# Performance work log

Measured on AMD Instinct MI355X. Metric: run time of the kernel, lower is better.

The kernel has to match this reference:

```python
import jax, jax.numpy as jnp
import numpy as np

B, S, E, H = 8, 1024, 1024, 16
D = E // H


def setup_inputs() -> dict:
    key = jax.random.key(0)
    ks = jax.random.split(key, 5)
    s = 1.0 / np.sqrt(E)
    return {
        "hidden_states": jax.random.normal(ks[0], (B, S, E), dtype=jnp.float32),
        "w_q": jax.random.normal(ks[1], (E, E), dtype=jnp.float32) * s,
        "w_k": jax.random.normal(ks[2], (E, E), dtype=jnp.float32) * s,
        "w_v": jax.random.normal(ks[3], (E, E), dtype=jnp.float32) * s,
        "w_out": jax.random.normal(ks[4], (E, E), dtype=jnp.float32) * s,
        "b_out": jnp.zeros((E,), dtype=jnp.float32),
    }


def reference(hidden_states, w_q, w_k, w_v, w_out, b_out):
    b, s = hidden_states.shape[0], hidden_states.shape[1]
    # Linear projections (weights stored as [in, out] = torch W^T)
    q = hidden_states @ w_q
    k = hidden_states @ w_k
    v = hidden_states @ w_v
    # Faithful to the original: raw reshape (B,S,E)->(B,H,S,D), NOT a head-split transpose
    q = q.reshape(b, H, s, D)
    k = k.reshape(b, H, s, D)
    v = v.reshape(b, H, s, D)
    # Scores scaled by embedding_size**-0.5 (original quirk, not head_dim**-0.5)
    scores = jnp.einsum("bhsd,bhtd->bhst", q, k) * (E ** -0.5)
    attn = jax.nn.softmax(scores, axis=-1)
    out = jnp.einsum("bhst,bhtd->bhsd", attn, v)  # [B,H,S,D]
    out = out.transpose(0, 2, 1, 3).reshape(b, s, E)  # [B,S,E]
    return out @ w_out + b_out
```

## Files before the change

### kernel.cpp

```cpp
#include <hip/hip_runtime.h>
#include <hip/hip_bf16.h>
#include <stdint.h>
#include <stddef.h>

static constexpr int Bb = 8, Ss = 1024, Ee = 1024, Hh = 16, Dd = 64;
static constexpr int Mm = Bb * Ss;

typedef __attribute__((ext_vector_type(8))) short frag8;
typedef __attribute__((ext_vector_type(4))) float fx4;
typedef __attribute__((ext_vector_type(4))) short s4v;

#define GP(p) ((const __attribute__((address_space(1))) void*)(p))
#define LP(p) ((__attribute__((address_space(3))) void*)(p))

static constexpr float QSC = 0.045084220027780106f;

__device__ inline short f2bf(float x) {
  union { float f; unsigned u; } c; c.f = x;
  unsigned u = c.u;
  unsigned r = (u + 0x7FFFu + ((u >> 16) & 1u)) >> 16;
  return (short)r;
}

__global__ __launch_bounds__(256) void cvt_kernel(const float* __restrict__ in,
                                                  short* __restrict__ out, int n4) {
  int i = blockIdx.x * 256 + threadIdx.x;
  if (i >= n4) return;
  float4 v = *((const float4*)in + i);
  union { short s[4]; uint2 u; } o;
  o.s[0] = f2bf(v.x); o.s[1] = f2bf(v.y); o.s[2] = f2bf(v.z); o.s[3] = f2bf(v.w);
  *(uint2*)(out + (size_t)i * 4) = o.u;
}

__global__ __launch_bounds__(256) void transpose_cvt4(const float* __restrict__ w0,
                                                      const float* __restrict__ w1,
                                                      const float* __restrict__ w2,
                                                      const float* __restrict__ w3,
                                                      short* __restrict__ WtBase) {
  __shared__ short tile[32][33];
  const int z = blockIdx.z;
  const float* W = z == 0 ? w0 : (z == 1 ? w1 : (z == 2 ? w2 : w3));
  short* Wt = WtBase + (size_t)z * 1024 * 1024;
  const int bx = blockIdx.x * 32;
  const int by = blockIdx.y * 32;
  const int tx = threadIdx.x & 31, ty = threadIdx.x >> 5;
  #pragma unroll
  for (int j = 0; j < 32; j += 8)
    tile[ty + j][tx] = f2bf(W[(size_t)(by + ty + j) * 1024 + bx + tx]);
  __syncthreads();
  #pragma unroll
  for (int j = 0; j < 32; j += 8)
    Wt[(size_t)(bx + ty + j) * 1024 + by + tx] = tile[tx][ty + j];
}

__global__ __launch_bounds__(256) void transpose_v(const short* __restrict__ V,
                                                   short* __restrict__ Vt) {
  __shared__ short tile[64][65];
  const int bh = blockIdx.y;
  const int s0 = blockIdx.x * 64;
  const short* Vb = V + (size_t)bh * 65536;
  short* Vtb = Vt + (size_t)bh * 65536;
  const int tx = threadIdx.x & 63, ty = threadIdx.x >> 6;
  #pragma unroll
  for (int j = 0; j < 64; j += 4)
    tile[ty + j][tx] = Vb[(size_t)(s0 + ty + j) * 64 + tx];
  __syncthreads();
  #pragma unroll
  for (int j = 0; j < 64; j += 4)
    Vtb[(size_t)(ty + j) * 1024 + s0 + tx] = tile[tx][ty + j];
}

template <int MODE>
__global__ __launch_bounds__(256) void gemm_bt(const short* __restrict__ A,
                                               const short* __restrict__ Bt,
                                               void* __restrict__ C0,
                                               void* __restrict__ C1,
                                               void* __restrict__ C2,
                                               const float* __restrict__ bias,
                                               int M, int N, int K) {
  __shared__ short As[128 * 32];
  __shared__ short Bs[128 * 32];
  const int t = threadIdx.x;
  const int w = t >> 6, lane = t & 63;
  const int fm = lane & 15, quad = lane >> 4;
  const int m0 = blockIdx.y * 128, n0 = blockIdx.x * 128;
  const int wm = (w >> 1) * 64, wn = (w & 1) * 64;
  fx4 acc[4][4];
  #pragma unroll
  for (int i = 0; i < 4; ++i)
    #pragma unroll
    for (int j = 0; j < 4; ++j) acc[i][j] = (fx4){0.f, 0.f, 0.f, 0.f};

  for (int k0 = 0; k0 < K; k0 += 32) {
    #pragma unroll
    for (int i = 0; i < 2; ++i) {
      int chunk = i * 256 + t;
      int row = chunk >> 2, cc = chunk & 3;
      __builtin_amdgcn_global_load_lds(GP(A + (size_t)(m0 + row) * K + k0 + cc * 8),
                                       LP(As + chunk * 8), 16, 0, 0);
      __builtin_amdgcn_global_load_lds(GP(Bt + (size_t)(n0 + row) * K + k0 + cc * 8),
                                       LP(Bs + chunk * 8), 16, 0, 0);
    }
    __syncthreads();
    frag8 af[4], bf[4];
    #pragma unroll
    for (int mt = 0; mt < 4; ++mt)
      af[mt] = *(const frag8*)(As + (wm + mt * 16 + fm) * 32 + quad * 8);
    #pragma unroll
    for (int nt = 0; nt < 4; ++nt)
      bf[nt] = *(const frag8*)(Bs + (wn + nt * 16 + fm) * 32 + quad * 8);
    #pragma unroll
    for (int mt = 0; mt < 4; ++mt)
      #pragma unroll
      for (int nt = 0; nt < 4; ++nt)
        acc[mt][nt] = __builtin_amdgcn_mfma_f32_16x16x32_bf16(af[mt], bf[nt], acc[mt][nt], 0, 0, 0);
    __syncthreads();
  }
  if (MODE == 0) {
    const int nb = n0 >> 10;
    short* dst = nb == 0 ? (short*)C0 : (nb == 1 ? (short*)C1 : (short*)C2);
    const float scl = (nb == 0) ? QSC : 1.0f;
    const int nl0 = n0 & 1023;
    #pragma unroll
    for (int mt = 0; mt < 4; ++mt)
      #pragma unroll
      for (int nt = 0; nt < 4; ++nt)
        #pragma unroll
        for (int r = 0; r < 4; ++r) {
          int row = m0 + wm + mt * 16 + quad * 4 + r;
          int col = nl0 + wn + nt * 16 + fm;
          dst[(size_t)row * 1024 + col] = f2bf(acc[mt][nt][r] * scl);
        }
  } else {
    #pragma unroll
    for (int mt = 0; mt < 4; ++mt)
      #pragma unroll
      for (int nt = 0; nt < 4; ++nt)
        #pragma unroll
        for (int r = 0; r < 4; ++r) {
          int row = m0 + wm + mt * 16 + quad * 4 + r;
          int col = n0 + wn + nt * 16 + fm;
          ((float*)C0)[(size_t)row * N + col] = acc[mt][nt][r] + bias[col];
        }
  }
}

__global__ __launch_bounds__(256, 2) void attn_kernel(const short* __restrict__ Q,
                                                      const short* __restrict__ K,
                                                      const short* __restrict__ Vt,
                                                      short* __restrict__ Ctx) {
  __shared__ short Ks[4096];
  __shared__ short Vs[4096];
  __shared__ short Plds[4 * 64 * 72];
  const int bh = blockIdx.x, qt = blockIdx.y;
  const int t = threadIdx.x;
  const int w = t >> 6, lane = t & 63;
  const int fm = lane & 15, quad = lane >> 4;
  const short* Qb = Q + (size_t)bh * 65536;
  const short* Kb = K + (size_t)bh * 65536;
  const short* Vb = Vt + (size_t)bh * 65536;
  const int q0 = qt * 256 + w * 64;
  short* myP = Plds + w * 4608;

  frag8 qb[4][2];
  #pragma unroll
  for (int g = 0; g < 4; ++g)
    #pragma unroll
    for (int h = 0; h < 2; ++h)
      qb[g][h] = *(const frag8*)(Qb + (size_t)(q0 + g * 16 + fm) * 64 + h * 32 + quad * 8);

  fx4 O[4][4];
  #pragma unroll
  for (int g = 0; g < 4; ++g)
    #pragma unroll
    for (int nt = 0; nt < 4; ++nt) O[g][nt] = (fx4){0.f, 0.f, 0.f, 0.f};
  float lp[4] = {0.f, 0.f, 0.f, 0.f};

  int koff[2], voff[2], loff[2];
  #pragma unroll
  for (int i = 0; i < 2; ++i) {
    int c = i * 256 + t;
    int cf = c & 15, cq = (c >> 4) & 3, ch = (c >> 6) & 1, cg = c >> 7;
    koff[i] = (cg * 16 + cf) * 64 + ch * 32 + cq * 8;
    voff[i] = (cg * 16 + cf) * 1024 + ch * 32 + cq * 8;
    loff[i] = c * 8;
  }

  for (int c = 0; c < 16; ++c) {
    const int key0 = c * 64;
    #pragma unroll
    for (int i = 0; i < 2; ++i) {
      __builtin_amdgcn_global_load_lds(GP(Kb + (size_t)key0 * 64 + koff[i]),
                                       LP(Ks + loff[i]), 16, 0, 0);
      __builtin_amdgcn_global_load_lds(GP(Vb + (size_t)key0 + voff[i]),
                                       LP(Vs + loff[i]), 16, 0, 0);
    }
    __syncthreads();

    #pragma unroll
    for (int s = 0; s < 4; ++s) {
      frag8 k0 = *(const frag8*)(Ks + (s * 2 + 0) * 512 + lane * 8);
      frag8 k1 = *(const frag8*)(Ks + (s * 2 + 1) * 512 + lane * 8);
      #pragma unroll
      for (int g = 0; g < 4; ++g) {
        fx4 z = (fx4){0.f, 0.f, 0.f, 0.f};
        z = __builtin_amdgcn_mfma_f32_16x16x32_bf16(k0, qb[g][0], z, 0, 0, 0);
        z = __builtin_amdgcn_mfma_f32_16x16x32_bf16(k1, qb[g][1], z, 0, 0, 0);
        s4v pv;
        #pragma unroll
        for (int r = 0; r < 4; ++r) {
          float p = __builtin_amdgcn_exp2f(z[r]);
          lp[g] += p;
          union { float f; unsigned u; } cv; cv.f = p;
          pv[r] = (short)(cv.u >> 16);
        }
        *(s4v*)(myP + (g * 16 + fm) * 72 + s * 16 + quad * 4) = pv;
      }
    }
    asm volatile("s_waitcnt lgkmcnt(0)" ::: "memory");
    #pragma unroll
    for (int h = 0; h < 2; ++h) {
      frag8 pf[4];
      #pragma unroll
      for (int g = 0; g < 4; ++g)
        pf[g] = *(const frag8*)(myP + (g * 16 + fm) * 72 + h * 32 + quad * 8);
      #pragma unroll
      for (int nt = 0; nt < 4; ++nt) {
        frag8 vf = *(const frag8*)(Vs + (nt * 2 + h) * 512 + lane * 8);
        #pragma unroll
        for (int g = 0; g < 4; ++g)
          O[g][nt] = __builtin_amdgcn_mfma_f32_16x16x32_bf16(pf[g], vf, O[g][nt], 0, 0, 0);
      }
    }
    __syncthreads();
  }

  float rl[4][4];
  #pragma unroll
  for (int g = 0; g < 4; ++g) {
    float v = lp[g];
    v += __shfl_xor(v, 16, 64);
    v += __shfl_xor(v, 32, 64);
    float inv = 1.f / v;
    #pragma unroll
    for (int r = 0; r < 4; ++r) rl[g][r] = __shfl(inv, quad * 4 + r, 16);
  }
  const int b = bh >> 4, h = bh & 15;
  #pragma unroll
  for (int g = 0; g < 4; ++g)
    #pragma unroll
    for (int nt = 0; nt < 4; ++nt)
      #pragma unroll
      for (int r = 0; r < 4; ++r) {
        int row = b * 1024 + q0 + g * 16 + quad * 4 + r;
        int col = h * 64 + nt * 16 + fm;
        Ctx[(size_t)row * 1024 + col] = f2bf(O[g][nt][r] * rl[g][r]);
      }
}

extern "C" void kernel_launch(void* const* d_in, const int* in_sizes, int n_in,
                              void* d_out, int out_size, void* d_ws, size_t ws_size,
                              hipStream_t stream) {
  const float* hs = (const float*)d_in[0];
  const float* wq = (const float*)d_in[1];
  const float* wk = (const float*)d_in[2];
  const float* wv = (const float*)d_in[3];
  const float* wo = (const float*)d_in[4];
  const float* bo = (const float*)d_in[5];
  float* out = (float*)d_out;

  char* wp = (char*)d_ws;
  const size_t MB16 = (size_t)Mm * Ee * 2;
  const size_t MB2  = (size_t)Ee * Ee * 2;
  short* Xb  = (short*)wp; wp += MB16;
  short* Wqt = (short*)wp; wp += MB2;
  short* Wkt = (short*)wp; wp += MB2;
  short* Wvt = (short*)wp; wp += MB2;
  short* Wot = (short*)wp; wp += MB2;
  short* Qb  = (short*)wp; wp += MB16;
  short* Kb  = (short*)wp; wp += MB16;
  short* Vb  = (short*)wp; wp += MB16;
  short* Vt  = (short*)wp; wp += MB16;
  short* Ctx = (short*)wp; wp += MB16;

  cvt_kernel<<<(Mm * Ee / 4 + 255) / 256, 256, 0, stream>>>(hs, Xb, Mm * Ee / 4);
  transpose_cvt4<<<dim3(32, 32, 4), 256, 0, stream>>>(wq, wk, wv, wo, Wqt);
  gemm_bt<0><<<dim3(24, 64), 256, 0, stream>>>(Xb, Wqt, Qb, Kb, Vb, nullptr, Mm, 3072, Ee);
  transpose_v<<<dim3(16, 128), 256, 0, stream>>>(Vb, Vt);
  attn_kernel<<<dim3(128, 4), 256, 0, stream>>>(Qb, Kb, Vt, Ctx);
  gemm_bt<1><<<dim3(8, 64), 256, 0, stream>>>(Ctx, Wot, out, nullptr, nullptr, bo, Mm, Ee, Ee);
}
```

Baseline: 249.4 us.

## Fuse prep kernels, write V transposed from GEMM epilogue, remap blocks per XCD

Merges the input conversion and weight transpose kernels into one launch, and removes the separate V transpose by having the QKV GEMM epilogue scatter V directly into the transposed layout used by attention. It also swizzles GEMM block indices so that each XCD handles a contiguous range of N tiles, which should improve L2 reuse of the weight tiles. The aim is to cut launch overhead and one full read/write pass over V. The trade-off is that the V stores in the epilogue are strided scatter writes, which coalesce less well.

After: 353.2 us. +41.6%, slower.

```diff
diff --git a/kernel.cpp b/kernel.cpp
--- a/kernel.cpp
+++ b/kernel.cpp
@@ -22,27 +22,29 @@
   return (short)r;
 }
 
-__global__ __launch_bounds__(256) void cvt_kernel(const float* __restrict__ in,
-                                                  short* __restrict__ out, int n4) {
-  int i = blockIdx.x * 256 + threadIdx.x;
-  if (i >= n4) return;
-  float4 v = *((const float4*)in + i);
-  union { short s[4]; uint2 u; } o;
-  o.s[0] = f2bf(v.x); o.s[1] = f2bf(v.y); o.s[2] = f2bf(v.z); o.s[3] = f2bf(v.w);
-  *(uint2*)(out + (size_t)i * 4) = o.u;
-}
-
-__global__ __launch_bounds__(256) void transpose_cvt4(const float* __restrict__ w0,
-                                                      const float* __restrict__ w1,
-                                                      const float* __restrict__ w2,
-                                                      const float* __restrict__ w3,
-                                                      short* __restrict__ WtBase) {
+__global__ __launch_bounds__(256) void prep_kernel(const float* __restrict__ hs,
+                                                   short* __restrict__ Xb,
+                                                   const float* __restrict__ w0,
+                                                   const float* __restrict__ w1,
+                                                   const float* __restrict__ w2,
+                                                   const float* __restrict__ w3,
+                                                   short* __restrict__ WtBase) {
   __shared__ short tile[32][33];
-  const int z = blockIdx.z;
+  const int id = blockIdx.x;
+  if (id < 8192) {
+    int i = id * 256 + threadIdx.x;
+    float4 v = *((const float4*)hs + i);
+    union { short s[4]; uint2 u; } o;
+    o.s[0] = f2bf(v.x); o.s[1] = f2bf(v.y); o.s[2] = f2bf(v.z); o.s[3] = f2bf(v.w);
+    *(uint2*)(Xb + (size_t)i * 4) = o.u;
+    return;
+  }
+  const int id2 = id - 8192;
+  const int z = id2 >> 10, t10 = id2 & 1023;
   const float* W = z == 0 ? w0 : (z == 1 ? w1 : (z == 2 ? w2 : w3));
   short* Wt = WtBase + (size_t)z * 1024 * 1024;
-  const int bx = blockIdx.x * 32;
-  const int by = blockIdx.y * 32;
+  const int bx = (t10 & 31) * 32;
+  const int by = (t10 >> 5) * 32;
   const int tx = threadIdx.x & 31, ty = threadIdx.x >> 5;
   #pragma unroll
   for (int j = 0; j < 32; j += 8)
@@ -51,23 +53,6 @@
   #pragma unroll
   for (int j = 0; j < 32; j += 8)
     Wt[(size_t)(bx + ty + j) * 1024 + by + tx] = tile[tx][ty + j];
-}
-
-__global__ __launch_bounds__(256) void transpose_v(const short* __restrict__ V,
-                                                   short* __restrict__ Vt) {
-  __shared__ short tile[64][65];
-  const int bh = blockIdx.y;
-  const int s0 = blockIdx.x * 64;
-  const short* Vb = V + (size_t)bh * 65536;
-  short* Vtb = Vt + (size_t)bh * 65536;
-  const int tx = threadIdx.x & 63, ty = threadIdx.x >> 6;
-  #pragma unroll
-  for (int j = 0; j < 64; j += 4)
-    tile[ty + j][tx] = Vb[(size_t)(s0 + ty + j) * 64 + tx];
-  __syncthreads();
-  #pragma unroll
-  for (int j = 0; j < 64; j += 4)
-    Vtb[(size_t)(ty + j) * 1024 + s0 + tx] = tile[tx][ty + j];
 }
 
 template <int MODE>
@@ -83,7 +68,10 @@
   const int t = threadIdx.x;
   const int w = t >> 6, lane = t & 63;
   const int fm = lane & 15, quad = lane >> 4;
-  const int m0 = blockIdx.y * 128, n0 = blockIdx.x * 128;
+  const int lin = blockIdx.x;
+  const int xcd = lin & 7, kk = lin >> 3;
+  const int m_t = kk & 63, nloc = kk >> 6;
+  const int m0 = m_t * 128, n0 = (xcd * (N >> 10) + nloc) * 128;
   const int wm = (w >> 1) * 64, wn = (w & 1) * 64;
   fx4 acc[4][4];
   #pragma unroll
@@ -118,19 +106,40 @@
   }
   if (MODE == 0) {
     const int nb = n0 >> 10;
-    short* dst = nb == 0 ? (short*)C0 : (nb == 1 ? (short*)C1 : (short*)C2);
-    const float scl = (nb == 0) ? QSC : 1.0f;
     const int nl0 = n0 & 1023;
-    #pragma unroll
-    for (int mt = 0; mt < 4; ++mt)
-      #pragma unroll
-      for (int nt = 0; nt < 4; ++nt)
-        #pragma unroll
-        for (int r = 0; r < 4; ++r) {
-          int row = m0 + wm + mt * 16 + quad * 4 + r;
-          int col = nl0 + wn + nt * 16 + fm;
-          dst[(size_t)row * 1024 + col] = f2bf(acc[mt][nt][r] * scl);
+    if (nb == 2) {
+      short* Vt = (short*)C2;
+      #pragma unroll
+      for (int mt = 0; mt < 4; ++mt) {
+        const int row = m0 + wm + mt * 16 + quad * 4;
+        const int b = row >> 10;
+        const int h = (row >> 6) & 15;
+        const int s_low = row & 63;
+        #pragma unroll
+        for (int nt = 0; nt < 4; ++nt) {
+          const int e = nl0 + wn + nt * 16 + fm;
+          const int d = e & 63;
+          const int sp_hi = e >> 6;
+          const size_t base = (size_t)(b * 16 + h) * 65536 + (size_t)d * 1024 + sp_hi;
+          #pragma unroll
+          for (int r = 0; r < 4; ++r)
+            Vt[base + (size_t)(s_low + r) * 16] = f2bf(acc[mt][nt][r]);
         }
+      }
+    } else {
+      short* dst = nb == 0 ? (short*)C0 : (short*)C1;
+      const float scl = (nb == 0) ? QSC : 1.0f;
+      #pragma unroll
+      for (int mt = 0; mt < 4; ++mt)
+        #pragma unroll
+        for (int nt = 0; nt < 4; ++nt)
+          #pragma unroll
+          for (int r = 0; r < 4; ++r) {
+            int row = m0 + wm + mt * 16 + quad * 4 + r;
+            int col = nl0 + wn + nt * 16 + fm;
+            dst[(size_t)row * 1024 + col] = f2bf(acc[mt][nt][r] * scl);
+          }
+    }
   } else {
     #pragma unroll
     for (int mt = 0; mt < 4; ++mt)
@@ -279,14 +288,12 @@
   short* Wot = (short*)wp; wp += MB2;
   short* Qb  = (short*)wp; wp += MB16;
   short* Kb  = (short*)wp; wp += MB16;
-  short* Vb  = (short*)wp; wp += MB16;
   short* Vt  = (short*)wp; wp += MB16;
   short* Ctx = (short*)wp; wp += MB16;
-
-  cvt_kernel<<<(Mm * Ee / 4 + 255) / 256, 256, 0, stream>>>(hs, Xb, Mm * Ee / 4);
-  transpose_cvt4<<<dim3(32, 32, 4), 256, 0, stream>>>(wq, wk, wv, wo, Wqt);
-  gemm_bt<0><<<dim3(24, 64), 256, 0, stream>>>(Xb, Wqt, Qb, Kb, Vb, nullptr, Mm, 3072, Ee);
-  transpose_v<<<dim3(16, 128), 256, 0, stream>>>(Vb, Vt);
+  (void)Wkt; (void)Wvt;
+
+  prep_kernel<<<12288, 256, 0, stream>>>(hs, Xb, wq, wk, wv, wo, Wqt);
+  gemm_bt<0><<<1536, 256, 0, stream>>>(Xb, Wqt, Qb, Kb, Vt, nullptr, Mm, 3072, Ee);
   attn_kernel<<<dim3(128, 4), 256, 0, stream>>>(Qb, Kb, Vt, Ctx);
-  gemm_bt<1><<<dim3(8, 64), 256, 0, stream>>>(Ctx, Wot, out, nullptr, nullptr, bo, Mm, Ee, Ee);
-}
+  gemm_bt<1><<<512, 256, 0, stream>>>(Ctx, Wot, out, nullptr, nullptr, bo, Mm, Ee, Ee);
+}
```

## Fuse input/weight prep kernels and remap GEMM blocks for XCD-aware locality

Applied to the files above, without the earlier changes.

Merges the activation fp32-to-bf16 conversion and the four weight transpose-conversions into one launch, removing a kernel launch and its tail. Switches both GEMMs to a 1D grid whose block index is remapped so blocks sharing the same N columns land on the same XCD (blockIdx mod 8), aiming to improve L2 reuse of weight tiles across the chiplets. The remap assumes N is a multiple of 8192/1024 per XCD and that M equals 8192, which ties it to these shapes.

Measured after the change: 252.6 us. About the same (+1.3%).

```diff
diff --git a/kernel.cpp b/kernel.cpp
--- a/kernel.cpp
+++ b/kernel.cpp
@@ -22,27 +22,29 @@
   return (short)r;
 }
 
-__global__ __launch_bounds__(256) void cvt_kernel(const float* __restrict__ in,
-                                                  short* __restrict__ out, int n4) {
-  int i = blockIdx.x * 256 + threadIdx.x;
-  if (i >= n4) return;
-  float4 v = *((const float4*)in + i);
-  union { short s[4]; uint2 u; } o;
-  o.s[0] = f2bf(v.x); o.s[1] = f2bf(v.y); o.s[2] = f2bf(v.z); o.s[3] = f2bf(v.w);
-  *(uint2*)(out + (size_t)i * 4) = o.u;
-}
-
-__global__ __launch_bounds__(256) void transpose_cvt4(const float* __restrict__ w0,
-                                                      const float* __restrict__ w1,
-                                                      const float* __restrict__ w2,
-                                                      const float* __restrict__ w3,
-                                                      short* __restrict__ WtBase) {
+__global__ __launch_bounds__(256) void prep_kernel(const float* __restrict__ hs,
+                                                   short* __restrict__ Xb,
+                                                   const float* __restrict__ w0,
+                                                   const float* __restrict__ w1,
+                                                   const float* __restrict__ w2,
+                                                   const float* __restrict__ w3,
+                                                   short* __restrict__ WtBase) {
   __shared__ short tile[32][33];
-  const int z = blockIdx.z;
+  const int id = blockIdx.x;
+  if (id < 8192) {
+    int i = id * 256 + threadIdx.x;
+    float4 v = *((const float4*)hs + i);
+    union { short s[4]; uint2 u; } o;
+    o.s[0] = f2bf(v.x); o.s[1] = f2bf(v.y); o.s[2] = f2bf(v.z); o.s[3] = f2bf(v.w);
+    *(uint2*)(Xb + (size_t)i * 4) = o.u;
+    return;
+  }
+  const int id2 = id - 8192;
+  const int z = id2 >> 10, t10 = id2 & 1023;
   const float* W = z == 0 ? w0 : (z == 1 ? w1 : (z == 2 ? w2 : w3));
   short* Wt = WtBase + (size_t)z * 1024 * 1024;
-  const int bx = blockIdx.x * 32;
-  const int by = blockIdx.y * 32;
+  const int bx = (t10 & 31) * 32;
+  const int by = (t10 >> 5) * 32;
   const int tx = threadIdx.x & 31, ty = threadIdx.x >> 5;
   #pragma unroll
   for (int j = 0; j < 32; j += 8)
@@ -83,7 +85,10 @@
   const int t = threadIdx.x;
   const int w = t >> 6, lane = t & 63;
   const int fm = lane & 15, quad = lane >> 4;
-  const int m0 = blockIdx.y * 128, n0 = blockIdx.x * 128;
+  const int lin = blockIdx.x;
+  const int xcd = lin & 7, kk = lin >> 3;
+  const int m_t = kk & 63, nloc = kk >> 6;
+  const int m0 = m_t * 128, n0 = (xcd * (N >> 10) + nloc) * 128;
   const int wm = (w >> 1) * 64, wn = (w & 1) * 64;
   fx4 acc[4][4];
   #pragma unroll
@@ -118,9 +123,9 @@
   }
   if (MODE == 0) {
     const int nb = n0 >> 10;
+    const int nl0 = n0 & 1023;
     short* dst = nb == 0 ? (short*)C0 : (nb == 1 ? (short*)C1 : (short*)C2);
     const float scl = (nb == 0) ? QSC : 1.0f;
-    const int nl0 = n0 & 1023;
     #pragma unroll
     for (int mt = 0; mt < 4; ++mt)
       #pragma unroll
@@ -282,11 +287,11 @@
   short* Vb  = (short*)wp; wp += MB16;
   short* Vt  = (short*)wp; wp += MB16;
   short* Ctx = (short*)wp; wp += MB16;
-
-  cvt_kernel<<<(Mm * Ee / 4 + 255) / 256, 256, 0, stream>>>(hs, Xb, Mm * Ee / 4);
-  transpose_cvt4<<<dim3(32, 32, 4), 256, 0, stream>>>(wq, wk, wv, wo, Wqt);
-  gemm_bt<0><<<dim3(24, 64), 256, 0, stream>>>(Xb, Wqt, Qb, Kb, Vb, nullptr, Mm, 3072, Ee);
+  (void)Wkt; (void)Wvt;
+
+  prep_kernel<<<12288, 256, 0, stream>>>(hs, Xb, wq, wk, wv, wo, Wqt);
+  gemm_bt<0><<<1536, 256, 0, stream>>>(Xb, Wqt, Qb, Kb, Vb, nullptr, Mm, 3072, Ee);
   transpose_v<<<dim3(16, 128), 256, 0, stream>>>(Vb, Vt);
   attn_kernel<<<dim3(128, 4), 256, 0, stream>>>(Qb, Kb, Vt, Ctx);
-  gemm_bt<1><<<dim3(8, 64), 256, 0, stream>>>(Ctx, Wot, out, nullptr, nullptr, bo, Mm, Ee, Ee);
-}
+  gemm_bt<1><<<512, 256, 0, stream>>>(Ctx, Wot, out, nullptr, nullptr, bo, Mm, Ee, Ee);
+}
```
